# Kernel optimization log

Measured on AMD Instinct MI355X. Metric: run time of the kernel, lower is better.

The kernel has to match this reference:

```python
import jax, jax.numpy as jnp
import numpy as np

N_DOMAIN = 10
DOM_EMB = 4
IN_DIM = 1024
HIDDEN = [1024, 512, 256]
N_EXPERTS = 8
LORA_R = 16


def _glorot(key, shape):
    fan_in, fan_out = shape[-2], shape[-1]
    lim = np.sqrt(6.0 / (fan_in + fan_out))
    return jax.random.uniform(key, shape, jnp.float32, -lim, lim)


def setup_inputs() -> dict:
    key = jax.random.key(0)
    ks = jax.random.split(key, 32)
    inp = {
        "dnn_input": jax.random.normal(ks[0], (16384, IN_DIM), jnp.float32),
        "domain_input": jax.random.randint(ks[1], (16384,), 0, N_DOMAIN, jnp.int64),
        "emb_table": jax.random.normal(ks[2], (N_DOMAIN, DOM_EMB), jnp.float32),
        "gate_W": _glorot(ks[3], (DOM_EMB, N_EXPERTS)),
        "gate_b": jnp.zeros((N_EXPERTS,), jnp.float32),
    }
    prev = IN_DIM
    k = 4
    for li, h in enumerate(HIDDEN):
        inp[f"W{li}"] = _glorot(ks[k], (prev, h)); k += 1
        inp[f"b{li}"] = jnp.zeros((h,), jnp.float32)
        # original inits B and lora_bias to zeros; use small randoms so outputs/grads are non-trivial
        inp[f"A{li}"] = _glorot(ks[k], (N_EXPERTS, prev, LORA_R)); k += 1
        inp[f"B{li}"] = 0.01 * jax.random.normal(ks[k], (N_EXPERTS, LORA_R, h), jnp.float32); k += 1
        inp[f"lb{li}"] = 0.01 * jax.random.normal(ks[k], (N_EXPERTS, h), jnp.float32); k += 1
        prev = h
    return inp


def _moe_layer(x, gate, W, b, A, B, lb):
    # base GEMM (dropout is identity: rate 0 / inference)
    base = x @ W + b                                   # [B, h]
    t = jnp.einsum('bp,epr->ber', x, A)                # [B, E, r]
    eo = jnp.einsum('ber,erh->beh', t, B) + lb[None]   # [B, E, h]
    moe = jnp.einsum('be,beh->bh', gate, eo)           # [B, h]
    return jax.nn.relu(base + moe)


def reference(dnn_input, domain_input, emb_table, gate_W, gate_b,
              W0, b0, A0, B0, lb0,
              W1, b1, A1, B1, lb1,
              W2, b2, A2, B2, lb2):
    dom = emb_table[domain_input]                      # [B, 4]
    gate = jax.nn.softmax(dom @ gate_W + gate_b, axis=-1)  # [B, E]
    x = dnn_input
    x = _moe_layer(x, gate, W0, b0, A0, B0, lb0)
    x = _moe_layer(x, gate, W1, b1, A1, B1, lb1)
    x = _moe_layer(x, gate, W2, b2, A2, B2, lb2)
    return x
```

## Files before the change

kernel.cpp:

```cpp
#include <hip/hip_runtime.h>
#include <hip/hip_bf16.h>
#include <stdint.h>

#define KAUG 192
#define M_ROWS 16384

typedef __attribute__((ext_vector_type(8))) __bf16 bf16x8;
typedef __attribute__((ext_vector_type(4))) float f32x4;

__device__ __forceinline__ unsigned short f2b(float f) {
  unsigned int u = __builtin_bit_cast(unsigned int, f);
  u = (u + 0x7fffu + ((u >> 16) & 1u)) >> 16;
  return (unsigned short)u;
}

__device__ __forceinline__ void lds_load16(const unsigned short* g, unsigned short* l) {
  __builtin_amdgcn_global_load_lds(
      (const __attribute__((address_space(1))) void*)g,
      (__attribute__((address_space(3))) void*)l, 16, 0, 0);
}

template<int N> __device__ __forceinline__ void vmcnt_wait() {
  if constexpr (N == 0)      asm volatile("s_waitcnt vmcnt(0)" ::: "memory");
  else if constexpr (N == 3) asm volatile("s_waitcnt vmcnt(3)" ::: "memory");
  else if constexpr (N == 4) asm volatile("s_waitcnt vmcnt(4)" ::: "memory");
  else if constexpr (N == 6) asm volatile("s_waitcnt vmcnt(6)" ::: "memory");
  else                       asm volatile("s_waitcnt vmcnt(8)" ::: "memory");
}


__global__ void gate_kernel(const int* __restrict__ dom, const float* __restrict__ emb,
                            const float* __restrict__ gW, const float* __restrict__ gb,
                            float* __restrict__ gate) {
  int i = blockIdx.x * blockDim.x + threadIdx.x;
  int d = dom[i];
  float e0 = emb[d*4+0], e1 = emb[d*4+1], e2 = emb[d*4+2], e3 = emb[d*4+3];
  float l[8]; float mx = -1e30f;
#pragma unroll
  for (int j = 0; j < 8; j++) {
    l[j] = e0*gW[j] + e1*gW[8+j] + e2*gW[16+j] + e3*gW[24+j] + gb[j];
    mx = fmaxf(mx, l[j]);
  }
  float s = 0.f;
#pragma unroll
  for (int j = 0; j < 8; j++) { l[j] = __expf(l[j] - mx); s += l[j]; }
  float inv = 1.0f / s;
#pragma unroll
  for (int j = 0; j < 8; j++) gate[i*8+j] = l[j] * inv;
}

__global__ void f32_to_bf16_vec(const float* __restrict__ in, unsigned short* __restrict__ out, int n4) {
  int i = blockIdx.x * blockDim.x + threadIdx.x;
  if (i >= n4) return;
  float4 v = ((const float4*)in)[i];
  ushort4 o;
  o.x = f2b(v.x); o.y = f2b(v.y); o.z = f2b(v.z); o.w = f2b(v.w);
  ((ushort4*)out)[i] = o;
}

__global__ void build_wt_t(const float* __restrict__ W, unsigned short* __restrict__ Wt,
                           int K, int N) {
  __shared__ float tl[32][33];
  int n0 = blockIdx.x * 32, k0 = blockIdx.y * 32;
  int tx = threadIdx.x & 31, ty = threadIdx.x >> 5;
#pragma unroll
  for (int i = 0; i < 32; i += 8)
    tl[ty + i][tx] = W[(long)(k0 + ty + i) * N + n0 + tx];
  __syncthreads();
#pragma unroll
  for (int i = 0; i < 32; i += 8)
    Wt[(long)(n0 + ty + i) * K + k0 + tx] = f2b(tl[tx][ty + i]);
}

__global__ void build_aft_t(const float* __restrict__ A, unsigned short* __restrict__ Aft, int P) {
  __shared__ float tl[64][17];
  int e = blockIdx.y; long p0 = (long)blockIdx.x * 64;
  int t = threadIdx.x;
#pragma unroll
  for (int pass = 0; pass < 4; pass++) {
    int idx = t + pass * 256;
    int pl = idx >> 4, r = idx & 15;
    tl[pl][r] = A[((long)e * P + p0 + pl) * 16 + r];
  }
  __syncthreads();
#pragma unroll
  for (int pass = 0; pass < 4; pass++) {
    int idx = t + pass * 256;
    int r = idx >> 6, pl = idx & 63;
    Aft[(long)(e * 16 + r) * P + p0 + pl] = f2b(tl[pl][r]);
  }
}

__global__ void build_bft_t(const float* __restrict__ Bm, const float* __restrict__ lb,
                            unsigned short* __restrict__ Bft, int H) {
  __shared__ float tl[32][33];
  int n0 = blockIdx.x * 32, kk0 = blockIdx.y * 32;
  int tx = threadIdx.x & 31, ty = threadIdx.x >> 5;
#pragma unroll
  for (int i = 0; i < 32; i += 8) {
    int kk = kk0 + ty + i;
    float v;
    if (kk < 128)       v = Bm[(long)kk * H + n0 + tx];
    else if (kk < 136)  v = lb[(long)(kk - 128) * H + n0 + tx];
    else                v = 0.f;
    tl[ty + i][tx] = v;
  }
  __syncthreads();
#pragma unroll
  for (int i = 0; i < 32; i += 8)
    Bft[(long)(n0 + ty + i) * KAUG + kk0 + tx] = f2b(tl[tx][ty + i]);
}

__global__ void aug_fill(const float* __restrict__ gate, unsigned short* __restrict__ tg) {
  int i = blockIdx.x * blockDim.x + threadIdx.x;
  int j = i & 63; int b = i >> 6;
  float v = (j < 8) ? gate[b*8 + j] : 0.f;
  tg[(long)b * KAUG + 128 + j] = f2b(v);
}

template<int MODE, int BM>
__global__ __launch_bounds__(512)
void gemm_mn(const unsigned short* __restrict__ A1, int lda1, int K1,
             const unsigned short* __restrict__ A2, int lda2, int K2,
             const unsigned short* __restrict__ Bt1, int ldb1,
             const unsigned short* __restrict__ Bt2, int ldb2,
             const float* __restrict__ bias,
             const float* __restrict__ gate,
             void* __restrict__ outp, int ldout) {
  constexpr int MFRAG = BM / 32;
  constexpr int ATOT = BM * 64;
  constexpr int BTOT = 128 * 64;
  constexpr int LA = BM / 64;
  constexpr int L = LA + 2;
  __shared__ __attribute__((aligned(16))) unsigned short lds[3 * ATOT + 3 * BTOT];

  const int t = threadIdx.x;
  const int lane = t & 63, wave = t >> 6;
  const int wr = wave >> 2, wc = wave & 3;
  const int rl = lane & 15, kg = lane >> 4;
  const int row0 = blockIdx.x * BM, col0 = blockIdx.y * 128;

  const int sr = t >> 3;
  const int sk = ((t & 7) ^ (sr & 7)) * 8;

  f32x4 acc[MFRAG][2];
#pragma unroll
  for (int m = 0; m < MFRAG; m++)
#pragma unroll
    for (int n = 0; n < 2; n++) acc[m][n] = (f32x4){0.f, 0.f, 0.f, 0.f};

  auto stageA = [&](int buf, int kt) {
    const unsigned short* src; long ld; int kl;
    if (kt < K1) { src = A1; ld = lda1; kl = kt; }
    else         { src = A2; ld = lda2; kl = kt - K1; }
    unsigned short* d = &lds[buf * ATOT + t * 8];
    const unsigned short* s = src + (long)(row0 + sr) * ld + kl + sk;
#pragma unroll
    for (int i = 0; i < LA; i++)
      lds_load16(s + (long)(i * 64) * ld, d + i * 4096);
  };
  auto stageB = [&](int buf, int kt) {
    const unsigned short* src; long ld; int kl;
    if (kt < K1) { src = Bt1; ld = ldb1; kl = kt; }
    else         { src = Bt2; ld = ldb2; kl = kt - K1; }
    unsigned short* d = &lds[3 * ATOT + buf * BTOT + t * 8];
    const unsigned short* s = src + (long)(col0 + sr) * ld + kl + sk;
    lds_load16(s, d);
    lds_load16(s + 64 * ld, d + 4096);
  };
  auto ldA = [&](int buf, int mg, int ks) {
    int lr = wr * (BM / 2) + mg * 16 + rl;
    int sc = (ks * 4 + kg) ^ (lr & 7);
    return *(const bf16x8*)&lds[buf * ATOT + lr * 64 + sc * 8];
  };
  auto ldB = [&](int buf, int n, int ks) {
    int cr = wc * 32 + n * 16 + rl;
    int sc = (ks * 4 + kg) ^ (cr & 7);
    return *(const bf16x8*)&lds[3 * ATOT + buf * BTOT + cr * 64 + sc * 8];
  };

  const int Ktot = K1 + K2;
  const int NT = Ktot / 64;

  stageA(0, 0); stageB(0, 0);
  stageA(1, 64); stageB(1, 64);
  vmcnt_wait<L>();
  __builtin_amdgcn_s_barrier();

  int bcur = 0;
  bf16x8 Bfv[2][2];
  for (int tt = 0; tt < NT; ++tt) {
    int bpf = bcur + 2; if (bpf > 2) bpf -= 3;
    const bool pf = (tt + 2 < NT);
    bf16x8 Af[(MFRAG + 1) / 2][2];
#pragma unroll
    for (int m = 0; m < MFRAG / 2; m++) { Af[m][0] = ldA(bcur, m, 0); Af[m][1] = ldA(bcur, m, 1); }
#pragma unroll
    for (int n = 0; n < 2; n++) { Bfv[n][0] = ldB(bcur, n, 0); Bfv[n][1] = ldB(bcur, n, 1); }
    if (pf) stageA(bpf, (tt + 2) * 64);
    __builtin_amdgcn_s_barrier();
    asm volatile("s_waitcnt lgkmcnt(0)" ::: "memory");
    __builtin_amdgcn_sched_barrier(0);
    __builtin_amdgcn_s_setprio(1);
#pragma unroll
    for (int m = 0; m < MFRAG / 2; m++)
#pragma unroll
      for (int n = 0; n < 2; n++) {
        acc[m][n] = __builtin_amdgcn_mfma_f32_16x16x32_bf16(Af[m][0], Bfv[n][0], acc[m][n], 0, 0, 0);
        acc[m][n] = __builtin_amdgcn_mfma_f32_16x16x32_bf16(Af[m][1], Bfv[n][1], acc[m][n], 0, 0, 0);
      }
    __builtin_amdgcn_s_setprio(0);
    __builtin_amdgcn_s_barrier();
#pragma unroll
    for (int m = 0; m < MFRAG / 2; m++) { Af[m][0] = ldA(bcur, MFRAG / 2 + m, 0); Af[m][1] = ldA(bcur, MFRAG / 2 + m, 1); }
    if (pf) stageB(bpf, (tt + 2) * 64);
    if (tt + 1 < NT) vmcnt_wait<L>();
    else             vmcnt_wait<0>();
    __builtin_amdgcn_s_barrier();
    asm volatile("s_waitcnt lgkmcnt(0)" ::: "memory");
    __builtin_amdgcn_sched_barrier(0);
    __builtin_amdgcn_s_setprio(1);
#pragma unroll
    for (int m = 0; m < MFRAG / 2; m++)
#pragma unroll
      for (int n = 0; n < 2; n++) {
        acc[MFRAG / 2 + m][n] = __builtin_amdgcn_mfma_f32_16x16x32_bf16(Af[m][0], Bfv[n][0], acc[MFRAG / 2 + m][n], 0, 0, 0);
        acc[MFRAG / 2 + m][n] = __builtin_amdgcn_mfma_f32_16x16x32_bf16(Af[m][1], Bfv[n][1], acc[MFRAG / 2 + m][n], 0, 0, 0);
      }
    __builtin_amdgcn_s_setprio(0);
    __builtin_amdgcn_s_barrier();
    bcur = bcur == 2 ? 0 : bcur + 1;
  }

#pragma unroll
  for (int m = 0; m < MFRAG; m++)
#pragma unroll
    for (int n = 0; n < 2; n++)
#pragma unroll
      for (int j = 0; j < 4; j++) {
        int row = row0 + wr * (BM / 2) + m * 16 + kg * 4 + j;
        int col = col0 + wc * 32 + n * 16 + rl;
        float v = acc[m][n][j];
        if (MODE == 0) {
          v *= gate[row * 8 + (col >> 4)];
          ((unsigned short*)outp)[(long)row * ldout + col] = f2b(v);
        } else {
          v += bias[col];
          v = fmaxf(v, 0.f);
          if (MODE == 1) ((unsigned short*)outp)[(long)row * ldout + col] = f2b(v);
          else           ((float*)outp)[(long)row * ldout + col] = v;
        }
      }
}

template<int MODE>
__global__ __launch_bounds__(512, 2)
void gemm8ph(const unsigned short* __restrict__ A1, int lda1, int K1,
             const unsigned short* __restrict__ A2, int lda2, int K2,
             const unsigned short* __restrict__ Bt1, int ldb1,
             const unsigned short* __restrict__ Bt2, int ldb2,
             const float* __restrict__ bias,
             void* __restrict__ outp, int ldout) {
  constexpr int AT = 256 * 64;
  __shared__ __attribute__((aligned(16))) unsigned short lds[4 * AT];

  const int t = threadIdx.x;
  const int lane = t & 63, wave = t >> 6;
  const int wr = wave >> 2, wc = wave & 3;
  const int rl = lane & 15, kg = lane >> 4;
  const int row0 = blockIdx.x * 256, col0 = blockIdx.y * 256;
  const int sr = t >> 3;
  const int sk = ((t & 7) ^ (sr & 7)) * 8;

  f32x4 acc[8][4];
#pragma unroll
  for (int m = 0; m < 8; m++)
#pragma unroll
    for (int n = 0; n < 4; n++) acc[m][n] = (f32x4){0.f, 0.f, 0.f, 0.f};

  auto stageHalf = [&](int buf, int isB, int rowOff, int tile) {
    int kt = tile * 64;
    const unsigned short* src; long ld; int kl;
    if (!isB) { if (kt < K1) { src = A1; ld = lda1; kl = kt; } else { src = A2; ld = lda2; kl = kt - K1; } }
    else      { if (kt < K1) { src = Bt1; ld = ldb1; kl = kt; } else { src = Bt2; ld = ldb2; kl = kt - K1; } }
    const int org = isB ? col0 : row0;
    unsigned short* d = &lds[(isB * 2 + buf) * AT + rowOff * 64 + t * 8];
    const unsigned short* s = src + (long)(org + rowOff + sr) * ld + kl + sk;
    lds_load16(s, d);
    lds_load16(s + 64 * ld, d + 4096);
  };

  bf16x8 Af[4][2], Bf[4][2];
  auto readA = [&](int buf, int mh) {
#pragma unroll
    for (int mf = 0; mf < 4; mf++) {
      int lr = wr * 128 + mh * 64 + mf * 16 + rl;
#pragma unroll
      for (int ks = 0; ks < 2; ks++)
        Af[mf][ks] = *(const bf16x8*)&lds[buf * AT + lr * 64 + (((ks * 4 + kg) ^ (lr & 7))) * 8];
    }
  };
  auto readB = [&](int buf, int nh) {
#pragma unroll
    for (int nfl = 0; nfl < 2; nfl++) {
      int cr = wc * 64 + (nh * 2 + nfl) * 16 + rl;
#pragma unroll
      for (int ks = 0; ks < 2; ks++)
        Bf[nh * 2 + nfl][ks] = *(const bf16x8*)&lds[(2 + buf) * AT + cr * 64 + (((ks * 4 + kg) ^ (cr & 7))) * 8];
    }
  };
  auto mmaQ = [&](int mh, int nh) {
    __builtin_amdgcn_s_setprio(1);
#pragma unroll
    for (int mf = 0; mf < 4; mf++)
#pragma unroll
      for (int nfl = 0; nfl < 2; nfl++) {
        acc[mh*4+mf][nh*2+nfl] = __builtin_amdgcn_mfma_f32_16x16x32_bf16(Af[mf][0], Bf[nh*2+nfl][0], acc[mh*4+mf][nh*2+nfl], 0, 0, 0);
        acc[mh*4+mf][nh*2+nfl] = __builtin_amdgcn_mfma_f32_16x16x32_bf16(Af[mf][1], Bf[nh*2+nfl][1], acc[mh*4+mf][nh*2+nfl], 0, 0, 0);
      }
    __builtin_amdgcn_s_setprio(0);
  };
#define BAR()  __builtin_amdgcn_s_barrier()
#define LGKM0() do { asm volatile("s_waitcnt lgkmcnt(0)" ::: "memory"); __builtin_amdgcn_sched_barrier(0); } while (0)

  const int NT = (K1 + K2) / 64;
  const int NH = (NT - 1) / 2;

  stageHalf(0, 1, 0, 0);  stageHalf(0, 1, 128, 0);
  stageHalf(0, 0, 0, 0);  stageHalf(0, 0, 128, 0);
  stageHalf(1, 1, 0, 1);  stageHalf(1, 1, 128, 1);
  stageHalf(1, 0, 0, 1);
  asm volatile("s_waitcnt vmcnt(6)" ::: "memory");
  BAR();

  for (int i = 0; i < NH; ++i) {
    const int tb = 2 * i;
    stageHalf(1, 0, 128, tb + 1);
    readA(0, 0); readB(0, 0);
    BAR(); LGKM0(); mmaQ(0, 0); BAR();
    readB(0, 1);
    BAR(); LGKM0(); mmaQ(0, 1); BAR();
    readA(0, 1);
    stageHalf(0, 1, 0, tb + 2);
    BAR(); LGKM0(); mmaQ(1, 0); BAR();
    stageHalf(0, 1, 128, tb + 2);
    stageHalf(0, 0, 0, tb + 2);
    asm volatile("s_waitcnt vmcnt(6)" ::: "memory");
    BAR(); mmaQ(1, 1); BAR();
    stageHalf(0, 0, 128, tb + 2);
    readA(1, 0); readB(1, 0);
    BAR(); LGKM0(); mmaQ(0, 0); BAR();
    readB(1, 1);
    BAR(); LGKM0(); mmaQ(0, 1); BAR();
    readA(1, 1);
    if (i < NH - 1) stageHalf(1, 1, 0, tb + 3);
    BAR(); LGKM0(); mmaQ(1, 0); BAR();
    if (i < NH - 1) { stageHalf(1, 1, 128, tb + 3); stageHalf(1, 0, 0, tb + 3); }
    asm volatile("s_waitcnt vmcnt(6)" ::: "memory");
    BAR(); mmaQ(1, 1); BAR();
  }

  asm volatile("s_waitcnt vmcnt(0)" ::: "memory");
  BAR();
  readA(0, 0); readB(0, 0); readB(0, 1);
  LGKM0();
  mmaQ(0, 0); mmaQ(0, 1);
  readA(0, 1);
  LGKM0();
  mmaQ(1, 0); mmaQ(1, 1);

#undef BAR
#undef LGKM0

#pragma unroll
  for (int m = 0; m < 8; m++)
#pragma unroll
    for (int n = 0; n < 4; n++)
#pragma unroll
      for (int j = 0; j < 4; j++) {
        int row = row0 + wr * 128 + m * 16 + kg * 4 + j;
        int col = col0 + wc * 64 + n * 16 + rl;
        float v = acc[m][n][j] + bias[col];
        v = fmaxf(v, 0.f);
        if (MODE == 1) ((unsigned short*)outp)[(long)row * ldout + col] = f2b(v);
        else           ((float*)outp)[(long)row * ldout + col] = v;
      }
}


extern "C" void kernel_launch(void* const* d_in, const int* in_sizes, int n_in,
                              void* d_out, int out_size, void* d_ws, size_t ws_size,
                              hipStream_t stream) {
  (void)in_sizes; (void)n_in; (void)out_size; (void)ws_size;
  const float* dnn = (const float*)d_in[0];
  const int*   dom = (const int*)d_in[1];
  const float* emb = (const float*)d_in[2];
  const float* gW  = (const float*)d_in[3];
  const float* gb  = (const float*)d_in[4];
  const float* Wm[3]  = {(const float*)d_in[5],  (const float*)d_in[10], (const float*)d_in[15]};
  const float* bm[3]  = {(const float*)d_in[6],  (const float*)d_in[11], (const float*)d_in[16]};
  const float* Am[3]  = {(const float*)d_in[7],  (const float*)d_in[12], (const float*)d_in[17]};
  const float* Bm[3]  = {(const float*)d_in[8],  (const float*)d_in[13], (const float*)d_in[18]};
  const float* lbm[3] = {(const float*)d_in[9],  (const float*)d_in[14], (const float*)d_in[19]};

  const int M = M_ROWS;
  const int dIn[3]  = {1024, 1024, 512};
  const int dOutN[3] = {1024, 512, 256};

  char* p = (char*)d_ws;
  auto carve = [&](size_t bytes) { char* r = p; p += (bytes + 255) & ~(size_t)255; return r; };
  float* gate = (float*)carve((size_t)M * 8 * sizeof(float));
  unsigned short* xb0 = (unsigned short*)carve((size_t)M * 1024 * 2);
  unsigned short* xb1 = (unsigned short*)carve((size_t)M * 1024 * 2);
  unsigned short* tg  = (unsigned short*)carve((size_t)M * KAUG * 2);
  unsigned short *Wt[3], *Aft[3], *Bft[3];
  for (int l = 0; l < 3; l++) {
    Wt[l]  = (unsigned short*)carve((size_t)dOutN[l] * dIn[l] * 2);
    Aft[l] = (unsigned short*)carve((size_t)128 * dIn[l] * 2);
    Bft[l] = (unsigned short*)carve((size_t)dOutN[l] * KAUG * 2);
  }

  gate_kernel<<<M / 256, 256, 0, stream>>>(dom, emb, gW, gb, gate);
  {
    int n4 = M * 1024 / 4;
    f32_to_bf16_vec<<<(n4 + 255) / 256, 256, 0, stream>>>(dnn, xb0, n4);
  }
  for (int l = 0; l < 3; l++) {
    build_wt_t<<<dim3(dOutN[l] / 32, dIn[l] / 32), 256, 0, stream>>>(Wm[l], Wt[l], dIn[l], dOutN[l]);
    build_aft_t<<<dim3(dIn[l] / 64, 8), 256, 0, stream>>>(Am[l], Aft[l], dIn[l]);
    build_bft_t<<<dim3(dOutN[l] / 32, KAUG / 32), 256, 0, stream>>>(Bm[l], lbm[l], Bft[l], dOutN[l]);
  }
  aug_fill<<<(M * 64) / 256, 256, 0, stream>>>(gate, tg);

  const unsigned short* xin = xb0;
  for (int l = 0; l < 3; l++) {
    int K1 = dIn[l], N = dOutN[l];
    gemm_mn<0, 64><<<dim3(M / 64, 1), 512, 0, stream>>>(
        xin, K1, K1, nullptr, 0, 0, Aft[l], K1, nullptr, 0, nullptr, gate, (void*)tg, KAUG);
    if (l == 0)
      gemm8ph<1><<<dim3(M / 256, N / 256), 512, 0, stream>>>(
          xin, K1, K1, tg, KAUG, KAUG, Wt[l], K1, Bft[l], KAUG, bm[l], (void*)xb1, N);
    else if (l == 1)
      gemm_mn<1, 256><<<dim3(M / 256, N / 128), 512, 0, stream>>>(
          xin, K1, K1, tg, KAUG, KAUG, Wt[l], K1, Bft[l], KAUG, bm[l], nullptr, (void*)xb0, N);
    else
      gemm_mn<2, 128><<<dim3(M / 128, N / 128), 512, 0, stream>>>(
          xin, K1, K1, tg, KAUG, KAUG, Wt[l], K1, Bft[l], KAUG, bm[l], nullptr, d_out, N);
    xin = (l == 0) ? xb1 : xb0;
  }
}
```

Baseline: 158.2 us.

## Replace layer-0 eight-phase GEMM with simpler 256x128 double-buffered kernel

Layer 0 now uses a new 4-wave kernel instead of the hand-scheduled 8-wave eight-phase kernel. The tile changes from 256x256 to 256x128 and the K step from 64 to 32, with a plain double-buffered loop and one barrier per K step. The aim is less barrier and phase overhead and more blocks in the grid. In exchange, each block reuses loaded data less and the loop no longer explicitly overlaps loads with MFMA work.

```diff
diff --git a/kernel.cpp b/kernel.cpp
--- a/kernel.cpp
+++ b/kernel.cpp
@@ -254,23 +254,25 @@
 }
 
 template<int MODE>
-__global__ __launch_bounds__(512, 2)
-void gemm8ph(const unsigned short* __restrict__ A1, int lda1, int K1,
-             const unsigned short* __restrict__ A2, int lda2, int K2,
-             const unsigned short* __restrict__ Bt1, int ldb1,
-             const unsigned short* __restrict__ Bt2, int ldb2,
-             const float* __restrict__ bias,
-             void* __restrict__ outp, int ldout) {
-  constexpr int AT = 256 * 64;
-  __shared__ __attribute__((aligned(16))) unsigned short lds[4 * AT];
+__global__ __launch_bounds__(256, 2)
+void gemm_w128(const unsigned short* __restrict__ A1, int lda1, int K1,
+               const unsigned short* __restrict__ A2, int lda2, int K2,
+               const unsigned short* __restrict__ Bt1, int ldb1,
+               const unsigned short* __restrict__ Bt2, int ldb2,
+               const float* __restrict__ bias,
+               void* __restrict__ outp, int ldout) {
+  constexpr int ATOT = 256 * 32;
+  constexpr int BTOT = 128 * 32;
+  __shared__ __attribute__((aligned(16))) unsigned short lds[2 * ATOT + 2 * BTOT];
 
   const int t = threadIdx.x;
   const int lane = t & 63, wave = t >> 6;
-  const int wr = wave >> 2, wc = wave & 3;
+  const int wr = wave >> 1, wc = wave & 1;
   const int rl = lane & 15, kg = lane >> 4;
-  const int row0 = blockIdx.x * 256, col0 = blockIdx.y * 256;
-  const int sr = t >> 3;
-  const int sk = ((t & 7) ^ (sr & 7)) * 8;
+  const int row0 = blockIdx.x * 256, col0 = blockIdx.y * 128;
+
+  const int sr = t >> 2;
+  const int sk = ((t & 3) ^ ((sr >> 1) & 3)) * 8;
 
   f32x4 acc[8][4];
 #pragma unroll
@@ -278,99 +280,57 @@
 #pragma unroll
     for (int n = 0; n < 4; n++) acc[m][n] = (f32x4){0.f, 0.f, 0.f, 0.f};
 
-  auto stageHalf = [&](int buf, int isB, int rowOff, int tile) {
-    int kt = tile * 64;
+  auto stageA = [&](int buf, int kt) {
     const unsigned short* src; long ld; int kl;
-    if (!isB) { if (kt < K1) { src = A1; ld = lda1; kl = kt; } else { src = A2; ld = lda2; kl = kt - K1; } }
-    else      { if (kt < K1) { src = Bt1; ld = ldb1; kl = kt; } else { src = Bt2; ld = ldb2; kl = kt - K1; } }
-    const int org = isB ? col0 : row0;
-    unsigned short* d = &lds[(isB * 2 + buf) * AT + rowOff * 64 + t * 8];
-    const unsigned short* s = src + (long)(org + rowOff + sr) * ld + kl + sk;
+    if (kt < K1) { src = A1; ld = lda1; kl = kt; }
+    else         { src = A2; ld = lda2; kl = kt - K1; }
+    unsigned short* d = &lds[buf * ATOT + t * 8];
+    const unsigned short* s = src + (long)(row0 + sr) * ld + kl + sk;
+#pragma unroll
+    for (int i = 0; i < 4; i++)
+      lds_load16(s + (long)(i * 64) * ld, d + i * 2048);
+  };
+  auto stageB = [&](int buf, int kt) {
+    const unsigned short* src; long ld; int kl;
+    if (kt < K1) { src = Bt1; ld = ldb1; kl = kt; }
+    else         { src = Bt2; ld = ldb2; kl = kt - K1; }
+    unsigned short* d = &lds[2 * ATOT + buf * BTOT + t * 8];
+    const unsigned short* s = src + (long)(col0 + sr) * ld + kl + sk;
     lds_load16(s, d);
-    lds_load16(s + 64 * ld, d + 4096);
-  };
-
-  bf16x8 Af[4][2], Bf[4][2];
-  auto readA = [&](int buf, int mh) {
-#pragma unroll
-    for (int mf = 0; mf < 4; mf++) {
-      int lr = wr * 128 + mh * 64 + mf * 16 + rl;
-#pragma unroll
-      for (int ks = 0; ks < 2; ks++)
-        Af[mf][ks] = *(const bf16x8*)&lds[buf * AT + lr * 64 + (((ks * 4 + kg) ^ (lr & 7))) * 8];
-    }
-  };
-  auto readB = [&](int buf, int nh) {
-#pragma unroll
-    for (int nfl = 0; nfl < 2; nfl++) {
-      int cr = wc * 64 + (nh * 2 + nfl) * 16 + rl;
-#pragma unroll
-      for (int ks = 0; ks < 2; ks++)
-        Bf[nh * 2 + nfl][ks] = *(const bf16x8*)&lds[(2 + buf) * AT + cr * 64 + (((ks * 4 + kg) ^ (cr & 7))) * 8];
-    }
-  };
-  auto mmaQ = [&](int mh, int nh) {
-    __builtin_amdgcn_s_setprio(1);
-#pragma unroll
-    for (int mf = 0; mf < 4; mf++)
-#pragma unroll
-      for (int nfl = 0; nfl < 2; nfl++) {
-        acc[mh*4+mf][nh*2+nfl] = __builtin_amdgcn_mfma_f32_16x16x32_bf16(Af[mf][0], Bf[nh*2+nfl][0], acc[mh*4+mf][nh*2+nfl], 0, 0, 0);
-        acc[mh*4+mf][nh*2+nfl] = __builtin_amdgcn_mfma_f32_16x16x32_bf16(Af[mf][1], Bf[nh*2+nfl][1], acc[mh*4+mf][nh*2+nfl], 0, 0, 0);
-      }
-    __builtin_amdgcn_s_setprio(0);
-  };
-#define BAR()  __builtin_amdgcn_s_barrier()
-#define LGKM0() do { asm volatile("s_waitcnt lgkmcnt(0)" ::: "memory"); __builtin_amdgcn_sched_barrier(0); } while (0)
-
-  const int NT = (K1 + K2) / 64;
-  const int NH = (NT - 1) / 2;
-
-  stageHalf(0, 1, 0, 0);  stageHalf(0, 1, 128, 0);
-  stageHalf(0, 0, 0, 0);  stageHalf(0, 0, 128, 0);
-  stageHalf(1, 1, 0, 1);  stageHalf(1, 1, 128, 1);
-  stageHalf(1, 0, 0, 1);
-  asm volatile("s_waitcnt vmcnt(6)" ::: "memory");
-  BAR();
-
-  for (int i = 0; i < NH; ++i) {
-    const int tb = 2 * i;
-    stageHalf(1, 0, 128, tb + 1);
-    readA(0, 0); readB(0, 0);
-    BAR(); LGKM0(); mmaQ(0, 0); BAR();
-    readB(0, 1);
-    BAR(); LGKM0(); mmaQ(0, 1); BAR();
-    readA(0, 1);
-    stageHalf(0, 1, 0, tb + 2);
-    BAR(); LGKM0(); mmaQ(1, 0); BAR();
-    stageHalf(0, 1, 128, tb + 2);
-    stageHalf(0, 0, 0, tb + 2);
-    asm volatile("s_waitcnt vmcnt(6)" ::: "memory");
-    BAR(); mmaQ(1, 1); BAR();
-    stageHalf(0, 0, 128, tb + 2);
-    readA(1, 0); readB(1, 0);
-    BAR(); LGKM0(); mmaQ(0, 0); BAR();
-    readB(1, 1);
-    BAR(); LGKM0(); mmaQ(0, 1); BAR();
-    readA(1, 1);
-    if (i < NH - 1) stageHalf(1, 1, 0, tb + 3);
-    BAR(); LGKM0(); mmaQ(1, 0); BAR();
-    if (i < NH - 1) { stageHalf(1, 1, 128, tb + 3); stageHalf(1, 0, 0, tb + 3); }
-    asm volatile("s_waitcnt vmcnt(6)" ::: "memory");
-    BAR(); mmaQ(1, 1); BAR();
-  }
-
-  asm volatile("s_waitcnt vmcnt(0)" ::: "memory");
-  BAR();
-  readA(0, 0); readB(0, 0); readB(0, 1);
-  LGKM0();
-  mmaQ(0, 0); mmaQ(0, 1);
-  readA(0, 1);
-  LGKM0();
-  mmaQ(1, 0); mmaQ(1, 1);
-
-#undef BAR
-#undef LGKM0
+    lds_load16(s + 64 * ld, d + 2048);
+  };
+  auto ldA = [&](int buf, int mf) {
+    int lr = wr * 128 + mf * 16 + rl;
+    int sc = kg ^ ((lr >> 1) & 3);
+    return *(const bf16x8*)&lds[buf * ATOT + lr * 32 + sc * 8];
+  };
+  auto ldB = [&](int buf, int nf) {
+    int cr = wc * 64 + nf * 16 + rl;
+    int sc = kg ^ ((cr >> 1) & 3);
+    return *(const bf16x8*)&lds[2 * ATOT + buf * BTOT + cr * 32 + sc * 8];
+  };
+
+  const int NT = (K1 + K2) / 32;
+
+  stageA(0, 0); stageB(0, 0);
+  __syncthreads();
+
+  int cur = 0;
+  for (int tt = 0; tt < NT; ++tt) {
+    if (tt + 1 < NT) { stageA(cur ^ 1, (tt + 1) * 32); stageB(cur ^ 1, (tt + 1) * 32); }
+    bf16x8 Af[8], Bf[4];
+#pragma unroll
+    for (int nf = 0; nf < 4; nf++) Bf[nf] = ldB(cur, nf);
+#pragma unroll
+    for (int mf = 0; mf < 8; mf++) Af[mf] = ldA(cur, mf);
+#pragma unroll
+    for (int mf = 0; mf < 8; mf++)
+#pragma unroll
+      for (int nf = 0; nf < 4; nf++)
+        acc[mf][nf] = __builtin_amdgcn_mfma_f32_16x16x32_bf16(Af[mf], Bf[nf], acc[mf][nf], 0, 0, 0);
+    __syncthreads();
+    cur ^= 1;
+  }
 
 #pragma unroll
   for (int m = 0; m < 8; m++)
@@ -438,7 +398,7 @@
     gemm_mn<0, 64><<<dim3(M / 64, 1), 512, 0, stream>>>(
         xin, K1, K1, nullptr, 0, 0, Aft[l], K1, nullptr, 0, nullptr, gate, (void*)tg, KAUG);
     if (l == 0)
-      gemm8ph<1><<<dim3(M / 256, N / 256), 512, 0, stream>>>(
+      gemm_w128<1><<<dim3(M / 256, N / 128), 256, 0, stream>>>(
           xin, K1, K1, tg, KAUG, KAUG, Wt[l], K1, Bft[l], KAUG, bm[l], (void*)xb1, N);
     else if (l == 1)
       gemm_mn<1, 256><<<dim3(M / 256, N / 128), 512, 0, stream>>>(
```

After: 162.2 us. 1.03x slower.
